# Performance work log

Hardware: AMD Instinct MI355X
Metric: run time of the kernel (lower is better)

The kernel has to match this reference:

```python
import jax, jax.numpy as jnp
import numpy as np

NUM_LAYERS = 4
EMBED = 1024
HEADS = 16
QKV = 1024
MLP = 4096
EPS_LN = 1e-6


def _layernorm(x, scale, bias):
    m = jnp.mean(x, axis=-1, keepdims=True)
    v = jnp.mean(jnp.square(x - m), axis=-1, keepdims=True)
    return (x - m) * jax.lax.rsqrt(v + EPS_LN) * scale + bias


def setup_inputs() -> dict:
    key = jax.random.key(0)
    ks = jax.random.split(key, 12)
    B, L = 4, 1024
    s = 0.02
    inp = {
        "queries": jax.random.normal(ks[0], (B, L, EMBED), dtype=jnp.float32),
        "Wq": jax.random.normal(ks[1], (NUM_LAYERS, EMBED, QKV), dtype=jnp.float32) * s,
        "bq": jnp.zeros((NUM_LAYERS, QKV), dtype=jnp.float32),
        "Wk": jax.random.normal(ks[2], (NUM_LAYERS, EMBED, QKV), dtype=jnp.float32) * s,
        "bk": jnp.zeros((NUM_LAYERS, QKV), dtype=jnp.float32),
        "Wv": jax.random.normal(ks[3], (NUM_LAYERS, EMBED, QKV), dtype=jnp.float32) * s,
        "bv": jnp.zeros((NUM_LAYERS, QKV), dtype=jnp.float32),
        "Wo": jax.random.normal(ks[4], (NUM_LAYERS, QKV, EMBED), dtype=jnp.float32) * s,
        "bo": jnp.zeros((NUM_LAYERS, EMBED), dtype=jnp.float32),
        "ln1_s": jnp.ones((NUM_LAYERS, EMBED), dtype=jnp.float32),
        "ln1_b": jnp.zeros((NUM_LAYERS, EMBED), dtype=jnp.float32),
        "ln2_s": jnp.ones((NUM_LAYERS, EMBED), dtype=jnp.float32),
        "ln2_b": jnp.zeros((NUM_LAYERS, EMBED), dtype=jnp.float32),
        "W1": jax.random.normal(ks[5], (NUM_LAYERS, EMBED, MLP), dtype=jnp.float32) * s,
        "b1": jnp.zeros((NUM_LAYERS, MLP), dtype=jnp.float32),
        "W2": jax.random.normal(ks[6], (NUM_LAYERS, MLP, EMBED), dtype=jnp.float32) * s,
        "b2": jnp.zeros((NUM_LAYERS, EMBED), dtype=jnp.float32),
    }
    return inp


def _block(x, Wq, bq, Wk, bk, Wv, bv, Wo, bo, ln1_s, ln1_b, ln2_s, ln2_b, W1, b1, W2, b2):
    # post-norm block (pre_norm=False)
    B, L, _ = x.shape
    head_dim = EMBED // HEADS
    q = (x @ Wq + bq).reshape(B, L, HEADS, head_dim)
    k = (x @ Wk + bk).reshape(B, L, HEADS, head_dim)
    v = (x @ Wv + bv).reshape(B, L, HEADS, head_dim)
    q = q / (head_dim ** 0.5)
    attn = jnp.einsum("bqhd,bkhd->bhqk", q, k)
    attn = jax.nn.softmax(attn, axis=-1)
    upd = jnp.einsum("bhqk,bkhd->bqhd", attn, v)  # [B,L,H,hd]
    a = upd.reshape(B, L, QKV) @ Wo + bo
    h = _layernorm(a + x, ln1_s, ln1_b)
    z = jax.nn.relu(h @ W1 + b1) @ W2 + b2
    return _layernorm(z + h, ln2_s, ln2_b)


def reference(queries, Wq, bq, Wk, bk, Wv, bv, Wo, bo, ln1_s, ln1_b, ln2_s, ln2_b, W1, b1, W2, b2):
    x = queries
    for l in range(NUM_LAYERS):
        x = _block(x, Wq[l], bq[l], Wk[l], bk[l], Wv[l], bv[l], Wo[l], bo[l],
                   ln1_s[l], ln1_b[l], ln2_s[l], ln2_b[l], W1[l], b1[l], W2[l], b2[l])
    return x
```

## Files before the change

### kernel.cpp

```cpp
#include <hip/hip_runtime.h>
#include <stdint.h>

typedef __bf16 bf16;
typedef __bf16 bf16x8 __attribute__((ext_vector_type(8)));
typedef float floatx4 __attribute__((ext_vector_type(4)));

#define LOG2E 1.44269504088896340736f

__device__ __forceinline__ void gl2lds16(const bf16* g, bf16* l) {
    __builtin_amdgcn_global_load_lds((__attribute__((address_space(1))) void*)g,
                                     (__attribute__((address_space(3))) void*)l,
                                     16, 0, 0);
}

template<int COLS>
__device__ __forceinline__ int swz(int ch, int r) {
    if constexpr (COLS == 32) return ch ^ ((r >> 1) & 3);
    else                      return ch ^ (r & 7);
}

template<int ROWS, int COLS>
__device__ __forceinline__ void stage_tile_sw(bf16* lds, const bf16* g, int srcStride, int wave, int lane) {
    constexpr int NINST = (ROWS * COLS * 2) / 1024;
    constexpr int ROWB  = COLS * 2;
    #pragma unroll
    for (int u = 0; u < NINST / 4; ++u) {
        int t  = wave + u * 4;
        int ob = t * 1024 + lane * 16;
        int r  = ob / ROWB;
        int ch = (ob % ROWB) >> 4;
        int sc = swz<COLS>(ch, r);
        gl2lds16(g + r * srcStride + sc * 8, lds + t * 512);
    }
}

template<int RELU, int OUTF, int OUTB>
__device__ __forceinline__ void gemm_core(const bf16* __restrict__ A, const bf16* __restrict__ Bt,
                                          const float* __restrict__ bias, float scale,
                                          float* __restrict__ outf, bf16* __restrict__ outb,
                                          int M, int N, int K, int m0, int n0) {
    __shared__ bf16 As[128 * 32];
    __shared__ bf16 Bs[128 * 32];
    const int tid = threadIdx.x, wave = tid >> 6, lane = tid & 63;
    const int wr = wave >> 1, wc = wave & 1;
    const int quad = lane >> 4, lq = lane & 15;
    const int swa = quad ^ ((lq >> 1) & 3);

    floatx4 acc[4][4] = {};
    const bf16* Ap = A + (size_t)m0 * K;
    const bf16* Bp = Bt + (size_t)n0 * K;

    for (int k0 = 0; k0 < K; k0 += 32) {
        stage_tile_sw<128, 32>(As, Ap + k0, K, wave, lane);
        stage_tile_sw<128, 32>(Bs, Bp + k0, K, wave, lane);
        __syncthreads();
        bf16x8 af[4], bfr[4];
        #pragma unroll
        for (int i = 0; i < 4; i++)
            af[i] = *(const bf16x8*)&As[(wr * 64 + i * 16 + lq) * 32 + swa * 8];
        #pragma unroll
        for (int j = 0; j < 4; j++)
            bfr[j] = *(const bf16x8*)&Bs[(wc * 64 + j * 16 + lq) * 32 + swa * 8];
        #pragma unroll
        for (int i = 0; i < 4; i++)
            #pragma unroll
            for (int j = 0; j < 4; j++)
                acc[i][j] = __builtin_amdgcn_mfma_f32_16x16x32_bf16(af[i], bfr[j], acc[i][j], 0, 0, 0);
        __syncthreads();
    }
    #pragma unroll
    for (int j = 0; j < 4; j++) {
        const int gc = n0 + wc * 64 + j * 16 + lq;
        const float bv = bias[gc];
        #pragma unroll
        for (int i = 0; i < 4; i++) {
            #pragma unroll
            for (int r = 0; r < 4; r++) {
                const int gr = m0 + wr * 64 + i * 16 + quad * 4 + r;
                float v = (acc[i][j][r] + bv) * scale;
                if (RELU) v = fmaxf(v, 0.f);
                if (OUTF) outf[(size_t)gr * N + gc] = v;
                if (OUTB) outb[(size_t)gr * N + gc] = (bf16)v;
            }
        }
    }
}

__global__ __launch_bounds__(256) void gemm_bf16relu(const bf16* A, const bf16* Bt, const float* bias,
                                                     bf16* out) {
    const int bid = blockIdx.x;
    const int xcd = bid & 7, j = bid >> 3;
    const int mt = xcd * 4 + (j >> 5);
    const int nt = j & 31;
    gemm_core<1, 0, 1>(A, Bt, bias, 1.f, nullptr, out, 4096, 4096, 1024, mt * 128, nt * 128);
}

__global__ __launch_bounds__(256) void gemm_qkv(const bf16* A, const bf16* Wt,
                                                const float* bq, const float* bk, const float* bv,
                                                bf16* out) {
    const int bid = blockIdx.x;
    const int xcd = bid & 7, j = bid >> 3;
    const int mloc = j / 24, r = j % 24;
    const int z = r >> 3, nt = r & 7;
    const int mt = xcd * 4 + mloc;
    const bf16* Bt = Wt + (size_t)z * 1024 * 1024;
    const float* bias = (z == 0) ? bq : (z == 1) ? bk : bv;
    bf16* o = out + (size_t)z * 4096 * 1024;
    const float scale = (z == 0) ? 0.125f * LOG2E : 1.f;
    gemm_core<0, 0, 1>(A, Bt, bias, scale, nullptr, o, 4096, 1024, 1024, mt * 128, nt * 128);
}

__global__ __launch_bounds__(256) void gemm_n1024(const bf16* __restrict__ A, const bf16* __restrict__ Bt,
                                                  const float* __restrict__ bias, float* __restrict__ out,
                                                  int K) {
    __shared__ bf16 As[128 * 64];
    __shared__ bf16 Bs[64 * 64];
    const int bid = blockIdx.x;
    const int xcd = bid & 7, j = bid >> 3;
    const int mt = xcd * 4 + (j >> 4);
    const int nt = j & 15;
    const int m0 = mt * 128, n0 = nt * 64;
    const int tid = threadIdx.x, wave = tid >> 6, lane = tid & 63;
    const int wr = wave >> 1, wc = wave & 1;
    const int quad = lane >> 4, lq = lane & 15;

    floatx4 acc[4][2] = {};
    const bf16* Ap = A + (size_t)m0 * K;
    const bf16* Bp = Bt + (size_t)n0 * K;

    for (int k0 = 0; k0 < K; k0 += 64) {
        stage_tile_sw<128, 64>(As, Ap + k0, K, wave, lane);
        stage_tile_sw<64, 64>(Bs, Bp + k0, K, wave, lane);
        __syncthreads();
        #pragma unroll
        for (int kk = 0; kk < 2; kk++) {
            const int chs = ((kk * 4 + quad) ^ (lq & 7)) * 8;
            bf16x8 af[4], bfr[2];
            #pragma unroll
            for (int i = 0; i < 4; i++)
                af[i] = *(const bf16x8*)&As[(wr * 64 + i * 16 + lq) * 64 + chs];
            #pragma unroll
            for (int jj = 0; jj < 2; jj++)
                bfr[jj] = *(const bf16x8*)&Bs[(wc * 32 + jj * 16 + lq) * 64 + chs];
            #pragma unroll
            for (int i = 0; i < 4; i++)
                #pragma unroll
                for (int jj = 0; jj < 2; jj++)
                    acc[i][jj] = __builtin_amdgcn_mfma_f32_16x16x32_bf16(af[i], bfr[jj], acc[i][jj], 0, 0, 0);
        }
        __syncthreads();
    }
    #pragma unroll
    for (int jj = 0; jj < 2; jj++) {
        const int gc = n0 + wc * 32 + jj * 16 + lq;
        const float bv = bias[gc];
        #pragma unroll
        for (int i = 0; i < 4; i++)
            #pragma unroll
            for (int r = 0; r < 4; r++) {
                const int gr = m0 + wr * 64 + i * 16 + quad * 4 + r;
                out[(size_t)gr * 1024 + gc] = acc[i][jj][r] + bv;
            }
    }
}

__device__ __forceinline__ void ttile(const float* __restrict__ src, bf16* __restrict__ dst,
                                      int K, int N, int n0, int k0) {
    __shared__ float t[32][33];
    const int tx = threadIdx.x & 31, ty = threadIdx.x >> 5;
    #pragma unroll
    for (int i = 0; i < 4; i++)
        t[ty + i * 8][tx] = src[(size_t)(k0 + ty + i * 8) * N + n0 + tx];
    __syncthreads();
    #pragma unroll
    for (int i = 0; i < 4; i++)
        dst[(size_t)(n0 + ty + i * 8) * K + k0 + tx] = (bf16)t[tx][ty + i * 8];
}

__global__ __launch_bounds__(256) void transpose_all(const float* Wq, const float* Wk, const float* Wv,
                                                     const float* Wo, const float* W1, const float* W2,
                                                     bf16* qkvT, bf16* oT, bf16* w1T, bf16* w2T) {
    const int bx = blockIdx.x;
    if (bx < 4096) {
        const int z = bx >> 10, tile = bx & 1023;
        const float* s = (z == 0) ? Wq : (z == 1) ? Wk : (z == 2) ? Wv : Wo;
        bf16* d = (z == 3) ? oT : qkvT + (size_t)z * 1048576;
        ttile(s, d, 1024, 1024, (tile & 31) * 32, (tile >> 5) * 32);
    } else if (bx < 8192) {
        const int tile = bx - 4096;
        ttile(W1, w1T, 1024, 4096, (tile & 127) * 32, (tile >> 7) * 32);
    } else {
        const int tile = bx - 8192;
        ttile(W2, w2T, 4096, 1024, (tile & 31) * 32, (tile >> 5) * 32);
    }
}

__global__ __launch_bounds__(256) void transpose_v(const bf16* v, bf16* vT) {
    __shared__ bf16 t[32][33];
    const int l0 = blockIdx.x * 32, d0 = blockIdx.y * 32, bh = blockIdx.z;
    const int b = bh >> 4, h = bh & 15;
    const int tx = threadIdx.x & 31, ty = threadIdx.x >> 5;
    #pragma unroll
    for (int i = 0; i < 4; i++)
        t[ty + i * 8][tx] = v[(size_t)(b * 1024 + l0 + ty + i * 8) * 1024 + h * 64 + d0 + tx];
    __syncthreads();
    #pragma unroll
    for (int i = 0; i < 4; i++)
        vT[((size_t)bh * 64 + d0 + ty + i * 8) * 1024 + l0 + tx] = t[tx][ty + i * 8];
}

__global__ __launch_bounds__(256) void cvt_f32_bf16(const float* src, bf16* dst) {
    const int i = (blockIdx.x * 256 + threadIdx.x) * 4;
    const float4 v = *(const float4*)(src + i);
    bf16 t4[4] = {(bf16)v.x, (bf16)v.y, (bf16)v.z, (bf16)v.w};
    *(uint64_t*)(dst + i) = *(const uint64_t*)t4;
}

__global__ __launch_bounds__(256) void ln_kernel(const float* __restrict__ a, const float* __restrict__ res,
                                                 const float* __restrict__ gamma, const float* __restrict__ beta,
                                                 float* __restrict__ outf, bf16* __restrict__ outb) {
    const int row = blockIdx.x, tid = threadIdx.x;
    const size_t base = (size_t)row * 1024 + tid * 4;
    const float4 av = *(const float4*)(a + base);
    const float4 rv = *(const float4*)(res + base);
    float x0 = av.x + rv.x, x1 = av.y + rv.y, x2 = av.z + rv.z, x3 = av.w + rv.w;
    float s  = x0 + x1 + x2 + x3;
    float sq = x0 * x0 + x1 * x1 + x2 * x2 + x3 * x3;
    #pragma unroll
    for (int off = 32; off; off >>= 1) {
        s  += __shfl_xor(s,  off, 64);
        sq += __shfl_xor(sq, off, 64);
    }
    __shared__ float red[8];
    const int wave = tid >> 6, lane = tid & 63;
    if (lane == 0) { red[wave] = s; red[wave + 4] = sq; }
    __syncthreads();
    const float S  = red[0] + red[1] + red[2] + red[3];
    const float SQ = red[4] + red[5] + red[6] + red[7];
    const float mean = S * (1.f / 1024.f);
    const float var  = SQ * (1.f / 1024.f) - mean * mean;
    const float rstd = rsqrtf(var + 1e-6f);
    const int c = tid * 4;
    const float4 g  = *(const float4*)(gamma + c);
    const float4 be = *(const float4*)(beta + c);
    float y0 = (x0 - mean) * rstd * g.x + be.x;
    float y1 = (x1 - mean) * rstd * g.y + be.y;
    float y2 = (x2 - mean) * rstd * g.z + be.z;
    float y3 = (x3 - mean) * rstd * g.w + be.w;
    float4 yo; yo.x = y0; yo.y = y1; yo.z = y2; yo.w = y3;
    *(float4*)(outf + base) = yo;
    bf16 t4[4] = {(bf16)y0, (bf16)y1, (bf16)y2, (bf16)y3};
    *(uint64_t*)(outb + base) = *(const uint64_t*)t4;
}

__global__ __launch_bounds__(256, 2) void attn_kernel(const bf16* __restrict__ Q, const bf16* __restrict__ Kg,
                                                      const bf16* __restrict__ Vt, bf16* __restrict__ O) {
    __shared__ bf16 Ks[128 * 64];
    __shared__ bf16 Vs[64 * 128];
    __shared__ bf16 Ps[128 * 128];
    const int bh = blockIdx.x, qt = blockIdx.y;
    const int b = bh >> 4, h = bh & 15;
    const int tid = threadIdx.x, wave = tid >> 6, lane = tid & 63;
    const int quad = lane >> 4, lq = lane & 15;

    const bf16* qg = Q + ((size_t)b * 1024 + qt * 128) * 1024 + h * 64;
    const bf16* kg = Kg + (size_t)b * 1024 * 1024 + h * 64;
    const bf16* vg = Vt + (size_t)bh * 64 * 1024;

    stage_tile_sw<128, 64>(Ps, qg, 1024, wave, lane);
    __syncthreads();
    bf16x8 aq[2][2];
    #pragma unroll
    for (int i = 0; i < 2; i++)
        #pragma unroll
        for (int kk = 0; kk < 2; kk++) {
            const int row = wave * 32 + i * 16 + lq;
            const int chs = (kk * 4 + quad) ^ (lq & 7);
            aq[i][kk] = *(const bf16x8*)&Ps[row * 64 + chs * 8];
        }

    floatx4 oacc[2][4] = {};
    float lsum[2][4] = {};

    for (int kt = 0; kt < 1024; kt += 128) {
        stage_tile_sw<128, 64>(Ks, kg + (size_t)kt * 1024, 1024, wave, lane);
        stage_tile_sw<64, 128>(Vs, vg + kt, 1024, wave, lane);
        __syncthreads();

        floatx4 sacc[2][8] = {};
        #pragma unroll
        for (int kk = 0; kk < 2; kk++)
            #pragma unroll
            for (int j = 0; j < 8; j++) {
                const int chs = (kk * 4 + quad) ^ (lq & 7);
                bf16x8 bk = *(const bf16x8*)&Ks[(j * 16 + lq) * 64 + chs * 8];
                sacc[0][j] = __builtin_amdgcn_mfma_f32_16x16x32_bf16(aq[0][kk], bk, sacc[0][j], 0, 0, 0);
                sacc[1][j] = __builtin_amdgcn_mfma_f32_16x16x32_bf16(aq[1][kk], bk, sacc[1][j], 0, 0, 0);
            }

        #pragma unroll
        for (int i = 0; i < 2; i++)
            #pragma unroll
            for (int r = 0; r < 4; r++) {
                const int row = wave * 32 + i * 16 + quad * 4 + r;
                const int rb = row & 7;
                float ls = 0.f;
                #pragma unroll
                for (int j = 0; j < 8; j++) {
                    const float pv = exp2f(sacc[i][j][r]);
                    ls += pv;
                    const int col = j * 16 + lq;
                    Ps[row * 128 + ((col >> 3) ^ rb) * 8 + (col & 7)] = (bf16)pv;
                }
                lsum[i][r] += ls;
            }

        #pragma unroll
        for (int kk = 0; kk < 4; kk++) {
            bf16x8 ap[2];
            #pragma unroll
            for (int i = 0; i < 2; i++) {
                const int row = wave * 32 + i * 16 + lq;
                const int chs = (kk * 4 + quad) ^ (lq & 7);
                ap[i] = *(const bf16x8*)&Ps[row * 128 + chs * 8];
            }
            #pragma unroll
            for (int dj = 0; dj < 4; dj++) {
                const int chs = (kk * 4 + quad) ^ (lq & 7);
                bf16x8 bv = *(const bf16x8*)&Vs[(dj * 16 + lq) * 128 + chs * 8];
                oacc[0][dj] = __builtin_amdgcn_mfma_f32_16x16x32_bf16(ap[0], bv, oacc[0][dj], 0, 0, 0);
                oacc[1][dj] = __builtin_amdgcn_mfma_f32_16x16x32_bf16(ap[1], bv, oacc[1][dj], 0, 0, 0);
            }
        }
        __syncthreads();
    }

    #pragma unroll
    for (int i = 0; i < 2; i++)
        #pragma unroll
        for (int r = 0; r < 4; r++) {
            float l = lsum[i][r];
            l += __shfl_xor(l, 1, 64); l += __shfl_xor(l, 2, 64);
            l += __shfl_xor(l, 4, 64); l += __shfl_xor(l, 8, 64);
            lsum[i][r] = 1.f / l;
        }
    #pragma unroll
    for (int i = 0; i < 2; i++)
        #pragma unroll
        for (int dj = 0; dj < 4; dj++)
            #pragma unroll
            for (int r = 0; r < 4; r++) {
                const int row = qt * 128 + wave * 32 + i * 16 + quad * 4 + r;
                O[((size_t)b * 1024 + row) * 1024 + h * 64 + dj * 16 + lq] = (bf16)(oacc[i][dj][r] * lsum[i][r]);
            }
}

extern "C" void kernel_launch(void* const* d_in, const int* in_sizes, int n_in,
                              void* d_out, int out_size, void* d_ws, size_t ws_size,
                              hipStream_t stream) {
    const float* queries = (const float*)d_in[0];
    const float* Wq = (const float*)d_in[1];  const float* bq = (const float*)d_in[2];
    const float* Wk = (const float*)d_in[3];  const float* bk = (const float*)d_in[4];
    const float* Wv = (const float*)d_in[5];  const float* bv = (const float*)d_in[6];
    const float* Wo = (const float*)d_in[7];  const float* bo = (const float*)d_in[8];
    const float* ln1_s = (const float*)d_in[9];   const float* ln1_b = (const float*)d_in[10];
    const float* ln2_s = (const float*)d_in[11];  const float* ln2_b = (const float*)d_in[12];
    const float* W1 = (const float*)d_in[13]; const float* b1 = (const float*)d_in[14];
    const float* W2 = (const float*)d_in[15]; const float* b2 = (const float*)d_in[16];

    char* p = (char*)d_ws;
    size_t off = 0;
    auto take = [&](size_t bytes) { void* r = p + off; off += bytes; return r; };
    bf16*  WqkvT = (bf16*)take(6291456);
    bf16*  WoT   = (bf16*)take(2097152);
    bf16*  W1T   = (bf16*)take(8388608);
    bf16*  W2T   = (bf16*)take(8388608);
    bf16*  x_bf  = (bf16*)take(8388608);
    float* xf    = (float*)take(16777216);
    bf16*  qkvb  = (bf16*)take(25165824);
    bf16*  vTb   = (bf16*)take(8388608);
    bf16*  updb  = (bf16*)take(8388608);
    float* az    = (float*)take(16777216);
    float* hf    = (float*)take(16777216);
    bf16*  hbf   = (bf16*)take(8388608);
    bf16*  tmlp  = (bf16*)take(33554432);

    cvt_f32_bf16<<<4096, 256, 0, stream>>>(queries, x_bf);

    for (int l = 0; l < 4; ++l) {
        const size_t w1k = (size_t)l * 1024 * 1024;
        const size_t w4m = (size_t)l * 4096 * 1024;
        transpose_all<<<12288, 256, 0, stream>>>(Wq + w1k, Wk + w1k, Wv + w1k, Wo + w1k,
                                                 W1 + w4m, W2 + w4m, WqkvT, WoT, W1T, W2T);

        gemm_qkv<<<768, 256, 0, stream>>>(x_bf, WqkvT,
                                          bq + l * 1024, bk + l * 1024, bv + l * 1024, qkvb);
        transpose_v<<<dim3(32, 2, 64), 256, 0, stream>>>(qkvb + 2 * 4194304, vTb);
        attn_kernel<<<dim3(64, 8), 256, 0, stream>>>(qkvb, qkvb + 4194304, vTb, updb);
        gemm_n1024<<<512, 256, 0, stream>>>(updb, WoT, bo + l * 1024, az, 1024);
        ln_kernel<<<4096, 256, 0, stream>>>(az, (l == 0) ? queries : xf,
                                            ln1_s + l * 1024, ln1_b + l * 1024, hf, hbf);
        gemm_bf16relu<<<1024, 256, 0, stream>>>(hbf, W1T, b1 + l * 4096, tmlp);
        gemm_n1024<<<512, 256, 0, stream>>>(tmlp, W2T, b2 + l * 1024, az, 4096);
        ln_kernel<<<4096, 256, 0, stream>>>(az, hf, ln2_s + l * 1024, ln2_b + l * 1024,
                                            (l == 3) ? (float*)d_out : xf, x_bf);
    }
}
```

Measured before the change: 1.158 ms.

## Use K=64 GEMM tiles, split-K for W2 GEMM, and hoist all weight transposes

The shared GEMM core now stages 64-wide K slices with an XOR swizzle, halving the number of barrier pairs per tile. The W2 projection switches from a 128x64 tile kernel to a 128x128 split-K kernel writing two partial fp32 outputs, which a new three-input layernorm sums. All four layers' weight transposes are merged into one launch before the layer loop, which removes per-layer launches but needs a larger workspace. The split-K path adds an extra fp32 intermediate read and write in exchange for better tile reuse.

```diff
diff --git a/kernel.cpp b/kernel.cpp
--- a/kernel.cpp
+++ b/kernel.cpp
@@ -35,43 +35,45 @@
 }
 
 template<int RELU, int OUTF, int OUTB>
-__device__ __forceinline__ void gemm_core(const bf16* __restrict__ A, const bf16* __restrict__ Bt,
-                                          const float* __restrict__ bias, float scale,
-                                          float* __restrict__ outf, bf16* __restrict__ outb,
-                                          int M, int N, int K, int m0, int n0) {
-    __shared__ bf16 As[128 * 32];
-    __shared__ bf16 Bs[128 * 32];
+__device__ __forceinline__ void gemm_core64(const bf16* __restrict__ Ap, const bf16* __restrict__ Bp,
+                                            int ld, int Kloop,
+                                            const float* __restrict__ bias, float scale,
+                                            float* __restrict__ outf, bf16* __restrict__ outb,
+                                            int N, int m0, int n0) {
+    __shared__ bf16 As[128 * 64];
+    __shared__ bf16 Bs[128 * 64];
     const int tid = threadIdx.x, wave = tid >> 6, lane = tid & 63;
     const int wr = wave >> 1, wc = wave & 1;
     const int quad = lane >> 4, lq = lane & 15;
-    const int swa = quad ^ ((lq >> 1) & 3);
 
     floatx4 acc[4][4] = {};
-    const bf16* Ap = A + (size_t)m0 * K;
-    const bf16* Bp = Bt + (size_t)n0 * K;
-
-    for (int k0 = 0; k0 < K; k0 += 32) {
-        stage_tile_sw<128, 32>(As, Ap + k0, K, wave, lane);
-        stage_tile_sw<128, 32>(Bs, Bp + k0, K, wave, lane);
-        __syncthreads();
-        bf16x8 af[4], bfr[4];
-        #pragma unroll
-        for (int i = 0; i < 4; i++)
-            af[i] = *(const bf16x8*)&As[(wr * 64 + i * 16 + lq) * 32 + swa * 8];
-        #pragma unroll
-        for (int j = 0; j < 4; j++)
-            bfr[j] = *(const bf16x8*)&Bs[(wc * 64 + j * 16 + lq) * 32 + swa * 8];
-        #pragma unroll
-        for (int i = 0; i < 4; i++)
+
+    for (int k0 = 0; k0 < Kloop; k0 += 64) {
+        stage_tile_sw<128, 64>(As, Ap + k0, ld, wave, lane);
+        stage_tile_sw<128, 64>(Bs, Bp + k0, ld, wave, lane);
+        __syncthreads();
+        #pragma unroll
+        for (int kk = 0; kk < 2; kk++) {
+            const int chs = ((kk * 4 + quad) ^ (lq & 7)) * 8;
+            bf16x8 af[4], bfr[4];
+            #pragma unroll
+            for (int i = 0; i < 4; i++)
+                af[i] = *(const bf16x8*)&As[(wr * 64 + i * 16 + lq) * 64 + chs];
             #pragma unroll
             for (int j = 0; j < 4; j++)
-                acc[i][j] = __builtin_amdgcn_mfma_f32_16x16x32_bf16(af[i], bfr[j], acc[i][j], 0, 0, 0);
+                bfr[j] = *(const bf16x8*)&Bs[(wc * 64 + j * 16 + lq) * 64 + chs];
+            #pragma unroll
+            for (int i = 0; i < 4; i++)
+                #pragma unroll
+                for (int j = 0; j < 4; j++)
+                    acc[i][j] = __builtin_amdgcn_mfma_f32_16x16x32_bf16(af[i], bfr[j], acc[i][j], 0, 0, 0);
+        }
         __syncthreads();
     }
     #pragma unroll
     for (int j = 0; j < 4; j++) {
         const int gc = n0 + wc * 64 + j * 16 + lq;
-        const float bv = bias[gc];
+        const float bv = bias ? bias[gc] : 0.f;
         #pragma unroll
         for (int i = 0; i < 4; i++) {
             #pragma unroll
@@ -92,7 +94,9 @@
     const int xcd = bid & 7, j = bid >> 3;
     const int mt = xcd * 4 + (j >> 5);
     const int nt = j & 31;
-    gemm_core<1, 0, 1>(A, Bt, bias, 1.f, nullptr, out, 4096, 4096, 1024, mt * 128, nt * 128);
+    const int m0 = mt * 128, n0 = nt * 128;
+    gemm_core64<1, 0, 1>(A + (size_t)m0 * 1024, Bt + (size_t)n0 * 1024, 1024, 1024,
+                         bias, 1.f, nullptr, out, 4096, m0, n0);
 }
 
 __global__ __launch_bounds__(256) void gemm_qkv(const bf16* A, const bf16* Wt,
@@ -102,12 +106,26 @@
     const int xcd = bid & 7, j = bid >> 3;
     const int mloc = j / 24, r = j % 24;
     const int z = r >> 3, nt = r & 7;
-    const int mt = xcd * 4 + mloc;
+    const int m0 = (xcd * 4 + mloc) * 128, n0 = nt * 128;
     const bf16* Bt = Wt + (size_t)z * 1024 * 1024;
     const float* bias = (z == 0) ? bq : (z == 1) ? bk : bv;
     bf16* o = out + (size_t)z * 4096 * 1024;
     const float scale = (z == 0) ? 0.125f * LOG2E : 1.f;
-    gemm_core<0, 0, 1>(A, Bt, bias, scale, nullptr, o, 4096, 1024, 1024, mt * 128, nt * 128);
+    gemm_core64<0, 0, 1>(A + (size_t)m0 * 1024, Bt + (size_t)n0 * 1024, 1024, 1024,
+                         bias, scale, nullptr, o, 1024, m0, n0);
+}
+
+__global__ __launch_bounds__(256) void gemm_splitk(const bf16* __restrict__ A, const bf16* __restrict__ Bt,
+                                                   const float* __restrict__ bias,
+                                                   float* __restrict__ out0, float* __restrict__ out1) {
+    const int bid = blockIdx.x;
+    const int xcd = bid & 7, j = bid >> 3;
+    const int mloc = j >> 4, rem = j & 15;
+    const int nt = rem >> 1, s = rem & 1;
+    const int m0 = (xcd * 4 + mloc) * 128, n0 = nt * 128;
+    const int ks = s * 2048;
+    gemm_core64<0, 1, 0>(A + (size_t)m0 * 4096 + ks, Bt + (size_t)n0 * 4096 + ks, 4096, 2048,
+                         s ? nullptr : bias, 1.f, s ? out1 : out0, nullptr, 1024, m0, n0);
 }
 
 __global__ __launch_bounds__(256) void gemm_n1024(const bf16* __restrict__ A, const bf16* __restrict__ Bt,
@@ -177,21 +195,25 @@
         dst[(size_t)(n0 + ty + i * 8) * K + k0 + tx] = (bf16)t[tx][ty + i * 8];
 }
 
-__global__ __launch_bounds__(256) void transpose_all(const float* Wq, const float* Wk, const float* Wv,
-                                                     const float* Wo, const float* W1, const float* W2,
-                                                     bf16* qkvT, bf16* oT, bf16* w1T, bf16* w2T) {
+#define WT_LAYER 12582912
+__global__ __launch_bounds__(256) void transpose_mega(const float* Wq, const float* Wk, const float* Wv,
+                                                      const float* Wo, const float* W1, const float* W2,
+                                                      bf16* WT) {
     const int bx = blockIdx.x;
-    if (bx < 4096) {
-        const int z = bx >> 10, tile = bx & 1023;
-        const float* s = (z == 0) ? Wq : (z == 1) ? Wk : (z == 2) ? Wv : Wo;
-        bf16* d = (z == 3) ? oT : qkvT + (size_t)z * 1048576;
+    const int l = bx / 12288, r = bx % 12288;
+    const size_t w1k = (size_t)l * 1048576, w4m = (size_t)l * 4194304;
+    bf16* base = WT + (size_t)l * WT_LAYER;
+    if (r < 4096) {
+        const int z = r >> 10, tile = r & 1023;
+        const float* s = (z == 0) ? Wq + w1k : (z == 1) ? Wk + w1k : (z == 2) ? Wv + w1k : Wo + w1k;
+        bf16* d = base + (size_t)z * 1048576;
         ttile(s, d, 1024, 1024, (tile & 31) * 32, (tile >> 5) * 32);
-    } else if (bx < 8192) {
-        const int tile = bx - 4096;
-        ttile(W1, w1T, 1024, 4096, (tile & 127) * 32, (tile >> 7) * 32);
+    } else if (r < 8192) {
+        const int tile = r - 4096;
+        ttile(W1 + w4m, base + 4194304, 1024, 4096, (tile & 127) * 32, (tile >> 7) * 32);
     } else {
-        const int tile = bx - 8192;
-        ttile(W2, w2T, 4096, 1024, (tile & 31) * 32, (tile >> 5) * 32);
+        const int tile = r - 8192;
+        ttile(W2 + w4m, base + 8388608, 4096, 1024, (tile & 31) * 32, (tile >> 5) * 32);
     }
 }
 
@@ -216,14 +238,20 @@
     *(uint64_t*)(dst + i) = *(const uint64_t*)t4;
 }
 
-__global__ __launch_bounds__(256) void ln_kernel(const float* __restrict__ a, const float* __restrict__ res,
-                                                 const float* __restrict__ gamma, const float* __restrict__ beta,
-                                                 float* __restrict__ outf, bf16* __restrict__ outb) {
+template<int NPART>
+__device__ __forceinline__ void ln_body(const float* __restrict__ a0, const float* __restrict__ a1,
+                                        const float* __restrict__ res,
+                                        const float* __restrict__ gamma, const float* __restrict__ beta,
+                                        float* __restrict__ outf, bf16* __restrict__ outb) {
     const int row = blockIdx.x, tid = threadIdx.x;
     const size_t base = (size_t)row * 1024 + tid * 4;
-    const float4 av = *(const float4*)(a + base);
+    const float4 av = *(const float4*)(a0 + base);
     const float4 rv = *(const float4*)(res + base);
     float x0 = av.x + rv.x, x1 = av.y + rv.y, x2 = av.z + rv.z, x3 = av.w + rv.w;
+    if (NPART == 2) {
+        const float4 bv = *(const float4*)(a1 + base);
+        x0 += bv.x; x1 += bv.y; x2 += bv.z; x3 += bv.w;
+    }
     float s  = x0 + x1 + x2 + x3;
     float sq = x0 * x0 + x1 * x1 + x2 * x2 + x3 * x3;
     #pragma unroll
@@ -253,6 +281,18 @@
     *(uint64_t*)(outb + base) = *(const uint64_t*)t4;
 }
 
+__global__ __launch_bounds__(256) void ln_kernel(const float* a, const float* res,
+                                                 const float* gamma, const float* beta,
+                                                 float* outf, bf16* outb) {
+    ln_body<1>(a, nullptr, res, gamma, beta, outf, outb);
+}
+
+__global__ __launch_bounds__(256) void ln3_kernel(const float* a0, const float* a1, const float* res,
+                                                  const float* gamma, const float* beta,
+                                                  float* outf, bf16* outb) {
+    ln_body<2>(a0, a1, res, gamma, beta, outf, outb);
+}
+
 __global__ __launch_bounds__(256, 2) void attn_kernel(const bf16* __restrict__ Q, const bf16* __restrict__ Kg,
                                                       const bf16* __restrict__ Vt, bf16* __restrict__ O) {
     __shared__ bf16 Ks[128 * 64];
@@ -371,38 +411,38 @@
     char* p = (char*)d_ws;
     size_t off = 0;
     auto take = [&](size_t bytes) { void* r = p + off; off += bytes; return r; };
-    bf16*  WqkvT = (bf16*)take(6291456);
-    bf16*  WoT   = (bf16*)take(2097152);
-    bf16*  W1T   = (bf16*)take(8388608);
-    bf16*  W2T   = (bf16*)take(8388608);
+    bf16*  WT    = (bf16*)take((size_t)4 * WT_LAYER * 2);
     bf16*  x_bf  = (bf16*)take(8388608);
     float* xf    = (float*)take(16777216);
     bf16*  qkvb  = (bf16*)take(25165824);
     bf16*  vTb   = (bf16*)take(8388608);
     bf16*  updb  = (bf16*)take(8388608);
-    float* az    = (float*)take(16777216);
+    float* az0   = (float*)take(16777216);
+    float* az1   = (float*)take(16777216);
     float* hf    = (float*)take(16777216);
     bf16*  hbf   = (bf16*)take(8388608);
     bf16*  tmlp  = (bf16*)take(33554432);
 
+    transpose_mega<<<49152, 256, 0, stream>>>(Wq, Wk, Wv, Wo, W1, W2, WT);
     cvt_f32_bf16<<<4096, 256, 0, stream>>>(queries, x_bf);
 
     for (int l = 0; l < 4; ++l) {
-        const size_t w1k = (size_t)l * 1024 * 1024;
-        const size_t w4m = (size_t)l * 4096 * 1024;
-        transpose_all<<<12288, 256, 0, stream>>>(Wq + w1k, Wk + w1k, Wv + w1k, Wo + w1k,
-                                                 W1 + w4m, W2 + w4m, WqkvT, WoT, W1T, W2T);
+        bf16* base  = WT + (size_t)l * WT_LAYER;
+        bf16* WqkvT = base;
+        bf16* WoT   = base + 3145728;
+        bf16* W1T   = base + 4194304;
+        bf16* W2T   = base + 8388608;
 
         gemm_qkv<<<768, 256, 0, stream>>>(x_bf, WqkvT,
                                           bq + l * 1024, bk + l * 1024, bv + l * 1024, qkvb);
         transpose_v<<<dim3(32, 2, 64), 256, 0, stream>>>(qkvb + 2 * 4194304, vTb);
         attn_kernel<<<dim3(64, 8), 256, 0, stream>>>(qkvb, qkvb + 4194304, vTb, updb);
-        gemm_n1024<<<512, 256, 0, stream>>>(updb, WoT, bo + l * 1024, az, 1024);
-        ln_kernel<<<4096, 256, 0, stream>>>(az, (l == 0) ? queries : xf,
+        gemm_n1024<<<512, 256, 0, stream>>>(updb, WoT, bo + l * 1024, az0, 1024);
+        ln_kernel<<<4096, 256, 0, stream>>>(az0, (l == 0) ? queries : xf,
                                             ln1_s + l * 1024, ln1_b + l * 1024, hf, hbf);
         gemm_bf16relu<<<1024, 256, 0, stream>>>(hbf, W1T, b1 + l * 4096, tmlp);
-        gemm_n1024<<<512, 256, 0, stream>>>(tmlp, W2T, b2 + l * 1024, az, 4096);
-        ln_kernel<<<4096, 256, 0, stream>>>(az, hf, ln2_s + l * 1024, ln2_b + l * 1024,
-                                            (l == 3) ? (float*)d_out : xf, x_bf);
-    }
-}
+        gemm_splitk<<<512, 256, 0, stream>>>(tmlp, W2T, b2 + l * 1024, az0, az1);
+        ln3_kernel<<<4096, 256, 0, stream>>>(az0, az1, hf, ln2_s + l * 1024, ln2_b + l * 1024,
+                                             (l == 3) ? (float*)d_out : xf, x_bf);
+    }
+}
```

Measured after the change: 1.236 ms. 1.07x slower.

## Merge per-layer weight transposes into one launch with 64x64 vectorized tiles

Applied to the files above, without the earlier changes.

Replaces the four per-layer weight transpose/convert launches with a single up-front kernel that transposes all layers' weights into a larger workspace. Each tile grows from 32x32 to 64x64, with float4 global reads and 16-byte bf16 stores instead of scalar accesses. This removes three launches and the serialization between each layer's transpose and its GEMMs, and is meant to raise memory efficiency of the conversion. It costs a workspace four times larger for the transposed weights, and the LDS writes are 2-byte scattered stores that may bank-conflict.

```diff
diff --git a/kernel.cpp b/kernel.cpp
--- a/kernel.cpp
+++ b/kernel.cpp
@@ -164,34 +164,52 @@
     }
 }
 
-__device__ __forceinline__ void ttile(const float* __restrict__ src, bf16* __restrict__ dst,
-                                      int K, int N, int n0, int k0) {
-    __shared__ float t[32][33];
-    const int tx = threadIdx.x & 31, ty = threadIdx.x >> 5;
-    #pragma unroll
-    for (int i = 0; i < 4; i++)
-        t[ty + i * 8][tx] = src[(size_t)(k0 + ty + i * 8) * N + n0 + tx];
+__device__ __forceinline__ void ttile64(const float* __restrict__ src, bf16* __restrict__ dst,
+                                        int K, int N, int n0, int k0) {
+    __shared__ bf16 Tl[64 * 68];
+    const int t = threadIdx.x;
+    const int nc = (t & 15) * 4;
+    const int kr = t >> 4;
+    #pragma unroll
+    for (int p = 0; p < 4; p++) {
+        const int kk = p * 16 + kr;
+        const float4 v = *(const float4*)(src + (size_t)(k0 + kk) * N + n0 + nc);
+        bf16 b4[4] = {(bf16)v.x, (bf16)v.y, (bf16)v.z, (bf16)v.w};
+        #pragma unroll
+        for (int j = 0; j < 4; j++)
+            Tl[(nc + j) * 68 + kk] = b4[j];
+    }
     __syncthreads();
-    #pragma unroll
-    for (int i = 0; i < 4; i++)
-        dst[(size_t)(n0 + ty + i * 8) * K + k0 + tx] = (bf16)t[tx][ty + i * 8];
-}
-
-__global__ __launch_bounds__(256) void transpose_all(const float* Wq, const float* Wk, const float* Wv,
-                                                     const float* Wo, const float* W1, const float* W2,
-                                                     bf16* qkvT, bf16* oT, bf16* w1T, bf16* w2T) {
+    const int kc = (t & 7) * 8;
+    #pragma unroll
+    for (int p = 0; p < 2; p++) {
+        const int nn = p * 32 + (t >> 3);
+        const bf16* rp = &Tl[nn * 68 + kc];
+        const uint2 a = *(const uint2*)rp;
+        const uint2 b = *(const uint2*)(rp + 4);
+        uint4 o; o.x = a.x; o.y = a.y; o.z = b.x; o.w = b.y;
+        *(uint4*)(dst + (size_t)(n0 + nn) * K + k0 + kc) = o;
+    }
+}
+
+#define WT_LAYER 12582912
+__global__ __launch_bounds__(256) void transpose_mega(const float* Wq, const float* Wk, const float* Wv,
+                                                      const float* Wo, const float* W1, const float* W2,
+                                                      bf16* WT) {
     const int bx = blockIdx.x;
-    if (bx < 4096) {
-        const int z = bx >> 10, tile = bx & 1023;
-        const float* s = (z == 0) ? Wq : (z == 1) ? Wk : (z == 2) ? Wv : Wo;
-        bf16* d = (z == 3) ? oT : qkvT + (size_t)z * 1048576;
-        ttile(s, d, 1024, 1024, (tile & 31) * 32, (tile >> 5) * 32);
-    } else if (bx < 8192) {
-        const int tile = bx - 4096;
-        ttile(W1, w1T, 1024, 4096, (tile & 127) * 32, (tile >> 7) * 32);
+    const int l = bx / 3072, r = bx % 3072;
+    const size_t w1k = (size_t)l * 1048576, w4m = (size_t)l * 4194304;
+    bf16* base = WT + (size_t)l * WT_LAYER;
+    if (r < 1024) {
+        const int z = r >> 8, tile = r & 255;
+        const float* s = (z == 0) ? Wq + w1k : (z == 1) ? Wk + w1k : (z == 2) ? Wv + w1k : Wo + w1k;
+        ttile64(s, base + (size_t)z * 1048576, 1024, 1024, (tile & 15) * 64, (tile >> 4) * 64);
+    } else if (r < 2048) {
+        const int tile = r - 1024;
+        ttile64(W1 + w4m, base + 4194304, 1024, 4096, (tile & 63) * 64, (tile >> 6) * 64);
     } else {
-        const int tile = bx - 8192;
-        ttile(W2, w2T, 4096, 1024, (tile & 31) * 32, (tile >> 5) * 32);
+        const int tile = r - 2048;
+        ttile64(W2 + w4m, base + 8388608, 4096, 1024, (tile & 15) * 64, (tile >> 4) * 64);
     }
 }
 
@@ -371,10 +389,7 @@
     char* p = (char*)d_ws;
     size_t off = 0;
     auto take = [&](size_t bytes) { void* r = p + off; off += bytes; return r; };
-    bf16*  WqkvT = (bf16*)take(6291456);
-    bf16*  WoT   = (bf16*)take(2097152);
-    bf16*  W1T   = (bf16*)take(8388608);
-    bf16*  W2T   = (bf16*)take(8388608);
+    bf16*  WT    = (bf16*)take((size_t)4 * WT_LAYER * 2);
     bf16*  x_bf  = (bf16*)take(8388608);
     float* xf    = (float*)take(16777216);
     bf16*  qkvb  = (bf16*)take(25165824);
@@ -385,13 +400,15 @@
     bf16*  hbf   = (bf16*)take(8388608);
     bf16*  tmlp  = (bf16*)take(33554432);
 
+    transpose_mega<<<12288, 256, 0, stream>>>(Wq, Wk, Wv, Wo, W1, W2, WT);
     cvt_f32_bf16<<<4096, 256, 0, stream>>>(queries, x_bf);
 
     for (int l = 0; l < 4; ++l) {
-        const size_t w1k = (size_t)l * 1024 * 1024;
-        const size_t w4m = (size_t)l * 4096 * 1024;
-        transpose_all<<<12288, 256, 0, stream>>>(Wq + w1k, Wk + w1k, Wv + w1k, Wo + w1k,
-                                                 W1 + w4m, W2 + w4m, WqkvT, WoT, W1T, W2T);
+        bf16* base  = WT + (size_t)l * WT_LAYER;
+        bf16* WqkvT = base;
+        bf16* WoT   = base + 3145728;
+        bf16* W1T   = base + 4194304;
+        bf16* W2T   = base + 8388608;
 
         gemm_qkv<<<768, 256, 0, stream>>>(x_bf, WqkvT,
                                           bq + l * 1024, bk + l * 1024, bv + l * 1024, qkvb);
```

New measurement: 1.252 ms. 8.1% more time.
